# Kernel optimization log

Hardware: AMD Instinct MI355X
Metric: run time of the kernel (lower is better)

The kernel has to match this reference:

```python
import jax, jax.numpy as jnp
import numpy as np

N_TOKENS = 16384
HIDDEN = 4096
N_EXPERTS = 64
TOP_K = 8


def setup_inputs() -> dict:
    key = jax.random.key(0)
    kx, kw, kb = jax.random.split(key, 3)
    x = jax.random.normal(kx, (N_TOKENS, HIDDEN), dtype=jnp.float32)
    # nn.Linear(hidden_dim, expert_num): weight [E, H], bias [E]
    W = jax.random.normal(kw, (N_EXPERTS, HIDDEN), dtype=jnp.float32) * (1.0 / np.sqrt(HIDDEN))
    b = jax.random.normal(kb, (N_EXPERTS,), dtype=jnp.float32) * 0.01
    return {"x": x, "W": W, "b": b}


def reference(x, W, b):
    # gate linear: [N, H] @ [H, E] + [E] -> [N, E]
    router = jnp.einsum("nh,eh->ne", x, W) + b
    # softmax over experts
    router_logits = jax.nn.softmax(router, axis=-1)
    # top-k over experts: values/indices [N, K]
    top_k_logits, top_k_indices = jax.lax.top_k(router_logits, TOP_K)
    # renormalize the selected probs
    router_weight = top_k_logits / jnp.sum(top_k_logits, axis=-1, keepdims=True)
    router_weight = router_weight.astype(x.dtype)
    # one-hot mask [N, K, E] -> permute(2,1,0) -> [E, K, N]
    expert_mask = jax.nn.one_hot(top_k_indices, N_EXPERTS, dtype=jnp.int32)
    expert_mask = jnp.transpose(expert_mask, (2, 1, 0))
    return (router, router_weight, top_k_indices, expert_mask)
```

## Files before the change

### kernel.cpp

```cpp
#include <hip/hip_runtime.h>

#define N_TOK 16384
#define HID   4096
#define N_EXP 64
#define TOPK  8

#define CH    64
#define NST   (HID / CH)

#define OFF_WT   (N_TOK * N_EXP)
#define OFF_IDX  (OFF_WT + N_TOK * TOPK)
#define OFF_MASK (OFF_IDX + N_TOK * TOPK)

typedef __attribute__((ext_vector_type(8))) _Float16 f16x8;
typedef __attribute__((ext_vector_type(4))) float f32x4;

static __device__ __forceinline__ void hsplit(float f, unsigned short &h, unsigned short &l)
{
    _Float16 hh = (_Float16)f;
    float r = f - (float)hh;
    _Float16 hl = (_Float16)r;
    h = __builtin_bit_cast(unsigned short, hh);
    l = __builtin_bit_cast(unsigned short, hl);
}

__global__ __launch_bounds__(256)
void prep_w(const float* __restrict__ W,
            unsigned short* __restrict__ wh, unsigned short* __restrict__ wl)
{
    const int i = blockIdx.x * 256 + threadIdx.x;
    float4 f = ((const float4*)W)[i];
    unsigned short h0,l0,h1,l1,h2,l2,h3,l3;
    hsplit(f.x,h0,l0); hsplit(f.y,h1,l1); hsplit(f.z,h2,l2); hsplit(f.w,h3,l3);
    *(uint2*)&wh[4*i] = make_uint2((unsigned)h0 | ((unsigned)h1<<16), (unsigned)h2 | ((unsigned)h3<<16));
    *(uint2*)&wl[4*i] = make_uint2((unsigned)l0 | ((unsigned)l1<<16), (unsigned)l2 | ((unsigned)l3<<16));
}

__global__ __launch_bounds__(256, 1)
void router_gemm(const float* __restrict__ x,
                 const unsigned short* __restrict__ wh,
                 const unsigned short* __restrict__ wl,
                 const float* __restrict__ b,
                 float* __restrict__ router)
{
    __shared__ unsigned short sXh[2][64 * CH];
    __shared__ unsigned short sXl[2][64 * CH];
    __shared__ unsigned short sWh[2][64 * CH];
    __shared__ unsigned short sWl[2][64 * CH];

    const int tid = threadIdx.x;
    const long t0 = (long)blockIdx.x * 64;

    const int xr0 = tid >> 4, xkq = tid & 15;
    const int wr0 = tid >> 3, wq  = tid & 7;

    const float*          xb  = x  + (t0 + xr0) * (long)HID + xkq * 4;
    const unsigned short* whb = wh + (long)wr0 * HID + wq * 8;
    const unsigned short* wlb = wl + (long)wr0 * HID + wq * 8;

    const int lane = tid & 63, wv = tid >> 6;
    const int wr = wv >> 1, wc = wv & 1;
    const int lrow = lane & 15, lg = lane >> 4, sw = lane & 7;

    float4 gx[4]; uint4 gwh[2], gwl[2];
    f32x4 acc[2][2] = {};

    auto LOAD = [&](int st) {
        const long o = (long)st * CH;
#pragma unroll
        for (int j = 0; j < 4; ++j)
            gx[j] = *(const float4*)(xb + (long)(16 * j) * HID + o);
#pragma unroll
        for (int j = 0; j < 2; ++j) {
            gwh[j] = *(const uint4*)(whb + (long)(32 * j) * HID + o);
            gwl[j] = *(const uint4*)(wlb + (long)(32 * j) * HID + o);
        }
    };

    auto STORE = [&](int buf) {
#pragma unroll
        for (int j = 0; j < 4; ++j) {
            const int r = xr0 + 16 * j;
            const int q = xkq >> 1;
            const int a = r * CH + (((q ^ (r & 7)) << 3) | ((xkq & 1) << 2));
            unsigned short h0,l0,h1,l1,h2,l2,h3,l3;
            hsplit(gx[j].x,h0,l0); hsplit(gx[j].y,h1,l1);
            hsplit(gx[j].z,h2,l2); hsplit(gx[j].w,h3,l3);
            *(uint2*)&sXh[buf][a] = make_uint2((unsigned)h0 | ((unsigned)h1<<16), (unsigned)h2 | ((unsigned)h3<<16));
            *(uint2*)&sXl[buf][a] = make_uint2((unsigned)l0 | ((unsigned)l1<<16), (unsigned)l2 | ((unsigned)l3<<16));
        }
#pragma unroll
        for (int j = 0; j < 2; ++j) {
            const int r = wr0 + 32 * j;
            const int a = r * CH + ((wq ^ (r & 7)) << 3);
            *(uint4*)&sWh[buf][a] = gwh[j];
            *(uint4*)&sWl[buf][a] = gwl[j];
        }
    };

    auto COMPUTE = [&](int buf) {
#pragma unroll
        for (int ks = 0; ks < CH / 32; ++ks) {
            f16x8 ah[2], al[2], bh[2], bl[2];
            const int qs = ((ks * 4 + lg) ^ sw) << 3;
#pragma unroll
            for (int ti = 0; ti < 2; ++ti) {
                const int a = (wr * 32 + ti * 16 + lrow) * CH + qs;
                ah[ti] = *(const f16x8*)&sXh[buf][a];
                al[ti] = *(const f16x8*)&sXl[buf][a];
            }
#pragma unroll
            for (int ei = 0; ei < 2; ++ei) {
                const int a = (wc * 32 + ei * 16 + lrow) * CH + qs;
                bh[ei] = *(const f16x8*)&sWh[buf][a];
                bl[ei] = *(const f16x8*)&sWl[buf][a];
            }
#pragma unroll
            for (int ti = 0; ti < 2; ++ti)
#pragma unroll
                for (int ei = 0; ei < 2; ++ei) {
                    acc[ti][ei] = __builtin_amdgcn_mfma_f32_16x16x32_f16(ah[ti], bh[ei], acc[ti][ei], 0, 0, 0);
                    acc[ti][ei] = __builtin_amdgcn_mfma_f32_16x16x32_f16(ah[ti], bl[ei], acc[ti][ei], 0, 0, 0);
                    acc[ti][ei] = __builtin_amdgcn_mfma_f32_16x16x32_f16(al[ti], bh[ei], acc[ti][ei], 0, 0, 0);
                }
        }
    };

    LOAD(0);
    STORE(0);
    __syncthreads();
#pragma unroll 1
    for (int st = 0; st < NST; ++st) {
        if (st + 1 < NST) LOAD(st + 1);
        COMPUTE(st & 1);
        if (st + 1 < NST) STORE((st + 1) & 1);
        __syncthreads();
    }

#pragma unroll
    for (int ei = 0; ei < 2; ++ei) {
        const int e = wc * 32 + ei * 16 + lrow;
        const float bias = b[e];
#pragma unroll
        for (int ti = 0; ti < 2; ++ti)
#pragma unroll
            for (int r = 0; r < 4; ++r) {
                const long tok = t0 + wr * 32 + ti * 16 + lg * 4 + r;
                router[tok * N_EXP + e] = acc[ti][ei][r] + bias;
            }
    }
}

__global__ __launch_bounds__(256)
void router_topk(const float* __restrict__ router, float* __restrict__ out)
{
    const int tid  = threadIdx.x;
    const int lane = tid & 63;
    const int wv   = tid >> 6;
    const int n    = blockIdx.x * 4 + wv;

    float l = router[(long)n * N_EXP + lane];

    float m = l;
#pragma unroll
    for (int o = 32; o > 0; o >>= 1) m = fmaxf(m, __shfl_xor(m, o));
    float p = expf(l - m);
    float Z = p;
#pragma unroll
    for (int o = 32; o > 0; o >>= 1) Z += __shfl_xor(Z, o);
    float prob = p / Z;

    float cur = prob;
    float myv = 0.f;
    int   myi = 0;
    float ssum = 0.f;
#pragma unroll
    for (int k = 0; k < TOPK; ++k) {
        float v = cur;
        int   id = lane;
#pragma unroll
        for (int o = 32; o > 0; o >>= 1) {
            float ov = __shfl_xor(v, o);
            int   oi = __shfl_xor(id, o);
            if (ov > v || (ov == v && oi < id)) { v = ov; id = oi; }
        }
        if (lane == k)  { myv = v; myi = id; }
        if (lane == id) cur = -1.f;
        ssum += v;
    }

    if (lane < TOPK) {
        out[OFF_WT  + (long)n * TOPK + lane] = myv / ssum;
        out[OFF_IDX + (long)n * TOPK + lane] = (float)myi;
    }
}

__global__ __launch_bounds__(256)
void mask_fill(const float* __restrict__ idxf, float* __restrict__ mask)
{
    const int bid = blockIdx.x;
    const int ek  = bid >> 2, qtr = bid & 3;
    const int k   = ek & 7;
    const float fe = (float)(ek >> 3);
    float* mbase = mask + (long)ek * N_TOK;
#pragma unroll
    for (int j = 0; j < 4; ++j) {
        const int n = qtr * 4096 + j * 1024 + threadIdx.x * 4;
        float4 v;
        v.x = (idxf[(long)(n + 0) * TOPK + k] == fe) ? 1.f : 0.f;
        v.y = (idxf[(long)(n + 1) * TOPK + k] == fe) ? 1.f : 0.f;
        v.z = (idxf[(long)(n + 2) * TOPK + k] == fe) ? 1.f : 0.f;
        v.w = (idxf[(long)(n + 3) * TOPK + k] == fe) ? 1.f : 0.f;
        *(float4*)&mbase[n] = v;
    }
}

extern "C" void kernel_launch(void* const* d_in, const int* in_sizes, int n_in,
                              void* d_out, int out_size, void* d_ws, size_t ws_size,
                              hipStream_t stream)
{
    const float* x = (const float*)d_in[0];
    const float* W = (const float*)d_in[1];
    const float* b = (const float*)d_in[2];
    float* out = (float*)d_out;

    unsigned short* wsh = (unsigned short*)d_ws;
    unsigned short* wsl = wsh + (size_t)N_EXP * HID;

    hipLaunchKernelGGL(prep_w,      dim3(N_EXP * HID / 1024), dim3(256), 0, stream, W, wsh, wsl);
    hipLaunchKernelGGL(router_gemm, dim3(N_TOK / 64),         dim3(256), 0, stream, x, wsh, wsl, b, out);
    hipLaunchKernelGGL(router_topk, dim3(N_TOK / 4),          dim3(256), 0, stream, out, out);
    hipLaunchKernelGGL(mask_fill,   dim3(N_EXP * TOPK * 4),   dim3(256), 0, stream,
                       out + OFF_IDX, out + OFF_MASK);
}
```

Measured before the change: 460.0 us.

## Replace LDS-staged GEMM with register-direct MFMA loads on smaller token tiles

The router GEMM no longer stages x and W tiles through shared memory. Each wave now loads its MFMA operands straight from global memory into registers, double-buffered in registers, and splits x into fp16 hi/lo parts in place. Blocks cover 16 tokens instead of 64, so there are four times as many blocks, and launch bounds allow four blocks per CU. This removes LDS traffic and barriers and raises occupancy to hide memory latency. In exchange, each x row is read by all four waves (served mostly from cache) and the W hi/lo data is fetched by every block, which raises L2 traffic.

```diff
diff --git a/kernel.cpp b/kernel.cpp
--- a/kernel.cpp
+++ b/kernel.cpp
@@ -4,9 +4,6 @@
 #define HID   4096
 #define N_EXP 64
 #define TOPK  8
-
-#define CH    64
-#define NST   (HID / CH)
 
 #define OFF_WT   (N_TOK * N_EXP)
 #define OFF_IDX  (OFF_WT + N_TOK * TOPK)
@@ -36,118 +33,78 @@
     *(uint2*)&wl[4*i] = make_uint2((unsigned)l0 | ((unsigned)l1<<16), (unsigned)l2 | ((unsigned)l3<<16));
 }
 
-__global__ __launch_bounds__(256, 1)
+__global__ __launch_bounds__(256, 4)
 void router_gemm(const float* __restrict__ x,
                  const unsigned short* __restrict__ wh,
                  const unsigned short* __restrict__ wl,
                  const float* __restrict__ b,
                  float* __restrict__ router)
 {
-    __shared__ unsigned short sXh[2][64 * CH];
-    __shared__ unsigned short sXl[2][64 * CH];
-    __shared__ unsigned short sWh[2][64 * CH];
-    __shared__ unsigned short sWl[2][64 * CH];
+    const int tid  = threadIdx.x;
+    const int lane = tid & 63, wv = tid >> 6;
+    const long t0  = (long)blockIdx.x * 16;
+    const int  e0  = wv * 16;
+    const int  lrow = lane & 15, lg = lane >> 4;
 
-    const int tid = threadIdx.x;
-    const long t0 = (long)blockIdx.x * 64;
+    const float*          xp  = x  + (t0 + lrow) * (long)HID + lg * 8;
+    const unsigned short* whp = wh + (long)(e0 + lrow) * HID + lg * 8;
+    const unsigned short* wlp = wl + (long)(e0 + lrow) * HID + lg * 8;
 
-    const int xr0 = tid >> 4, xkq = tid & 15;
-    const int wr0 = tid >> 3, wq  = tid & 7;
+    f32x4 acc = {};
 
-    const float*          xb  = x  + (t0 + xr0) * (long)HID + xkq * 4;
-    const unsigned short* whb = wh + (long)wr0 * HID + wq * 8;
-    const unsigned short* wlb = wl + (long)wr0 * HID + wq * 8;
+    auto LOAD = [&](int st, float4 (&xv)[4], uint4 (&hv)[2], uint4 (&lv)[2]) {
+        const long o = (long)st * 64;
+        xv[0] = *(const float4*)(xp + o);
+        xv[1] = *(const float4*)(xp + o + 4);
+        xv[2] = *(const float4*)(xp + o + 32);
+        xv[3] = *(const float4*)(xp + o + 36);
+        hv[0] = *(const uint4*)(whp + o);
+        hv[1] = *(const uint4*)(whp + o + 32);
+        lv[0] = *(const uint4*)(wlp + o);
+        lv[1] = *(const uint4*)(wlp + o + 32);
+    };
 
-    const int lane = tid & 63, wv = tid >> 6;
-    const int wr = wv >> 1, wc = wv & 1;
-    const int lrow = lane & 15, lg = lane >> 4, sw = lane & 7;
-
-    float4 gx[4]; uint4 gwh[2], gwl[2];
-    f32x4 acc[2][2] = {};
-
-    auto LOAD = [&](int st) {
-        const long o = (long)st * CH;
+    auto COMP = [&](const float4 (&xv)[4], const uint4 (&hv)[2], const uint4 (&lv)[2]) {
 #pragma unroll
-        for (int j = 0; j < 4; ++j)
-            gx[j] = *(const float4*)(xb + (long)(16 * j) * HID + o);
+        for (int ks = 0; ks < 2; ++ks) {
+            float xf[8];
+            *(float4*)&xf[0] = xv[2 * ks];
+            *(float4*)&xf[4] = xv[2 * ks + 1];
+            f16x8 ah, al;
 #pragma unroll
-        for (int j = 0; j < 2; ++j) {
-            gwh[j] = *(const uint4*)(whb + (long)(32 * j) * HID + o);
-            gwl[j] = *(const uint4*)(wlb + (long)(32 * j) * HID + o);
+            for (int j = 0; j < 8; ++j) {
+                _Float16 h = (_Float16)xf[j];
+                ah[j] = h;
+                al[j] = (_Float16)(xf[j] - (float)h);
+            }
+            const f16x8 bh = __builtin_bit_cast(f16x8, hv[ks]);
+            const f16x8 bl = __builtin_bit_cast(f16x8, lv[ks]);
+            acc = __builtin_amdgcn_mfma_f32_16x16x32_f16(ah, bh, acc, 0, 0, 0);
+            acc = __builtin_amdgcn_mfma_f32_16x16x32_f16(ah, bl, acc, 0, 0, 0);
+            acc = __builtin_amdgcn_mfma_f32_16x16x32_f16(al, bh, acc, 0, 0, 0);
         }
     };
 
-    auto STORE = [&](int buf) {
-#pragma unroll
-        for (int j = 0; j < 4; ++j) {
-            const int r = xr0 + 16 * j;
-            const int q = xkq >> 1;
-            const int a = r * CH + (((q ^ (r & 7)) << 3) | ((xkq & 1) << 2));
-            unsigned short h0,l0,h1,l1,h2,l2,h3,l3;
-            hsplit(gx[j].x,h0,l0); hsplit(gx[j].y,h1,l1);
-            hsplit(gx[j].z,h2,l2); hsplit(gx[j].w,h3,l3);
-            *(uint2*)&sXh[buf][a] = make_uint2((unsigned)h0 | ((unsigned)h1<<16), (unsigned)h2 | ((unsigned)h3<<16));
-            *(uint2*)&sXl[buf][a] = make_uint2((unsigned)l0 | ((unsigned)l1<<16), (unsigned)l2 | ((unsigned)l3<<16));
-        }
-#pragma unroll
-        for (int j = 0; j < 2; ++j) {
-            const int r = wr0 + 32 * j;
-            const int a = r * CH + ((wq ^ (r & 7)) << 3);
-            *(uint4*)&sWh[buf][a] = gwh[j];
-            *(uint4*)&sWl[buf][a] = gwl[j];
-        }
-    };
+    float4 xA[4], xB[4];
+    uint4  hA[2], hB[2], lA[2], lB[2];
 
-    auto COMPUTE = [&](int buf) {
-#pragma unroll
-        for (int ks = 0; ks < CH / 32; ++ks) {
-            f16x8 ah[2], al[2], bh[2], bl[2];
-            const int qs = ((ks * 4 + lg) ^ sw) << 3;
-#pragma unroll
-            for (int ti = 0; ti < 2; ++ti) {
-                const int a = (wr * 32 + ti * 16 + lrow) * CH + qs;
-                ah[ti] = *(const f16x8*)&sXh[buf][a];
-                al[ti] = *(const f16x8*)&sXl[buf][a];
-            }
-#pragma unroll
-            for (int ei = 0; ei < 2; ++ei) {
-                const int a = (wc * 32 + ei * 16 + lrow) * CH + qs;
-                bh[ei] = *(const f16x8*)&sWh[buf][a];
-                bl[ei] = *(const f16x8*)&sWl[buf][a];
-            }
-#pragma unroll
-            for (int ti = 0; ti < 2; ++ti)
-#pragma unroll
-                for (int ei = 0; ei < 2; ++ei) {
-                    acc[ti][ei] = __builtin_amdgcn_mfma_f32_16x16x32_f16(ah[ti], bh[ei], acc[ti][ei], 0, 0, 0);
-                    acc[ti][ei] = __builtin_amdgcn_mfma_f32_16x16x32_f16(ah[ti], bl[ei], acc[ti][ei], 0, 0, 0);
-                    acc[ti][ei] = __builtin_amdgcn_mfma_f32_16x16x32_f16(al[ti], bh[ei], acc[ti][ei], 0, 0, 0);
-                }
-        }
-    };
+    LOAD(0, xA, hA, lA);
+    LOAD(1, xB, hB, lB);
 
-    LOAD(0);
-    STORE(0);
-    __syncthreads();
 #pragma unroll 1
-    for (int st = 0; st < NST; ++st) {
-        if (st + 1 < NST) LOAD(st + 1);
-        COMPUTE(st & 1);
-        if (st + 1 < NST) STORE((st + 1) & 1);
-        __syncthreads();
+    for (int st = 0; st < HID / 64; st += 2) {
+        COMP(xA, hA, lA);
+        if (st + 2 < HID / 64) LOAD(st + 2, xA, hA, lA);
+        COMP(xB, hB, lB);
+        if (st + 3 < HID / 64) LOAD(st + 3, xB, hB, lB);
     }
 
+    const int e = e0 + lrow;
+    const float bias = b[e];
 #pragma unroll
-    for (int ei = 0; ei < 2; ++ei) {
-        const int e = wc * 32 + ei * 16 + lrow;
-        const float bias = b[e];
-#pragma unroll
-        for (int ti = 0; ti < 2; ++ti)
-#pragma unroll
-            for (int r = 0; r < 4; ++r) {
-                const long tok = t0 + wr * 32 + ti * 16 + lg * 4 + r;
-                router[tok * N_EXP + e] = acc[ti][ei][r] + bias;
-            }
+    for (int r = 0; r < 4; ++r) {
+        const long tok = t0 + lg * 4 + r;
+        router[tok * N_EXP + e] = acc[r] + bias;
     }
 }
 
@@ -228,7 +185,7 @@
     unsigned short* wsl = wsh + (size_t)N_EXP * HID;
 
     hipLaunchKernelGGL(prep_w,      dim3(N_EXP * HID / 1024), dim3(256), 0, stream, W, wsh, wsl);
-    hipLaunchKernelGGL(router_gemm, dim3(N_TOK / 64),         dim3(256), 0, stream, x, wsh, wsl, b, out);
+    hipLaunchKernelGGL(router_gemm, dim3(N_TOK / 16),         dim3(256), 0, stream, x, wsh, wsl, b, out);
     hipLaunchKernelGGL(router_topk, dim3(N_TOK / 4),          dim3(256), 0, stream, out, out);
     hipLaunchKernelGGL(mask_fill,   dim3(N_EXP * TOPK * 4),   dim3(256), 0, stream,
                        out + OFF_IDX, out + OFF_MASK);
```

Measured after the change: 541.7 us. 1.18x slower.
